# Kernel tuning notes

Hardware: AMD Instinct MI355X
Metric: run time of the kernel (lower is better)

The kernel has to match this reference:

```python
import jax, jax.numpy as jnp
import numpy as np

NINF = -1e5  # large negative used for forbidden transitions (as in partial-tagger)


def setup_inputs() -> dict:
    key = jax.random.key(0)
    ks = jax.random.split(key, 10)
    B, T, H, N = 64, 512, 768, 25
    embeddings = jax.random.normal(ks[0], (B, T, H), jnp.float32)
    lengths = jax.random.randint(ks[1], (B,), T // 2, T + 1)
    mask = jnp.arange(T)[None, :] < lengths[:, None]  # [B,T] bool
    W = jax.random.normal(ks[2], (H, N), jnp.float32) / np.sqrt(H).astype(np.float32)
    b = jnp.zeros((N,), jnp.float32)
    transitions = jax.random.normal(ks[3], (N, N), jnp.float32) * 0.1
    start_transitions = jax.random.normal(ks[4], (N,), jnp.float32) * 0.1
    end_transitions = jax.random.normal(ks[5], (N,), jnp.float32) * 0.1
    start_constraints = (jax.random.uniform(ks[6], (N,)) < 0.7).at[0].set(True)
    end_constraints = (jax.random.uniform(ks[7], (N,)) < 0.7).at[0].set(True)
    transition_constraints = (jax.random.uniform(ks[8], (N, N)) < 0.6) | jnp.eye(N, dtype=bool)
    return dict(embeddings=embeddings, W=W, b=b, transitions=transitions,
                start_transitions=start_transitions, end_transitions=end_transitions,
                mask=mask, start_constraints=start_constraints, end_constraints=end_constraints,
                transition_constraints=transition_constraints, padding_index=0)


def _log_potentials(embeddings, W, b, transitions, start_transitions, end_transitions, mask):
    # emissions [B,T,N]; lp[b,t,k,j] = emit[b,t,j] + trans[k,j]
    B, T, _ = embeddings.shape
    N = transitions.shape[0]
    logits = jnp.einsum('bth,hn->btn', embeddings, W) + b
    lp = logits[:, :, None, :] + transitions[None, None]  # [B,T,N,N]
    first = jnp.broadcast_to((start_transitions + logits[:, 0])[:, None, :], (B, N, N))
    lp = lp.at[:, 0].set(first)
    last_pos = mask.sum(-1) - 1  # [B]
    end_mask = jnp.arange(T)[None, :] == last_pos[:, None]  # [B,T]
    lp = lp + jnp.where(end_mask[:, :, None, None], end_transitions[None, None, None, :], 0.0)
    return lp


def _constrain(lp, mask, start_constraints, end_constraints, transition_constraints):
    B, T, N, _ = lp.shape
    tc = jnp.where(transition_constraints, 0.0, NINF)  # [N,N]
    sc = jnp.where(start_constraints, 0.0, NINF)       # [N]
    ec = jnp.where(end_constraints, 0.0, NINF)         # [N]
    clp = lp + tc[None, None]
    clp = clp.at[:, 0].set(lp[:, 0] + sc[None, None, :])  # start constraint, no transition constraint at t=0
    last_pos = mask.sum(-1) - 1
    end_mask = jnp.arange(T)[None, :] == last_pos[:, None]
    clp = clp + jnp.where(end_mask[:, :, None, None], ec[None, None, None, :], 0.0)
    # padded steps: force a 0-score self transition so they don't affect the path score
    eye = jnp.where(jnp.eye(N, dtype=bool), 0.0, NINF)
    clp = jnp.where(mask[:, :, None, None], clp, eye[None, None])
    return clp


def _viterbi(clp):
    # clp: [B,T,N,N] constrained log potentials -> best tag sequence [B,T]
    clp_t = jnp.swapaxes(clp, 0, 1)  # time-major [T,B,N,N]
    alpha0 = clp_t[0, :, 0, :]  # first-step rows are identical -> take row 0, [B,N]

    def fwd_step(alpha, lp_t):
        scores = alpha[:, :, None] + lp_t  # [B,N,N]
        return jnp.max(scores, axis=1), jnp.argmax(scores, axis=1).astype(jnp.int32)

    alpha_T, backptrs = jax.lax.scan(fwd_step, alpha0, clp_t[1:])  # backptrs [T-1,B,N]
    last_tag = jnp.argmax(alpha_T, axis=-1).astype(jnp.int32)  # [B]

    def bwd_step(tag, bp):
        prev = jnp.take_along_axis(bp, tag[:, None], axis=1).squeeze(1)
        return prev, prev

    _, prevs = jax.lax.scan(bwd_step, last_tag, backptrs, reverse=True)  # [T-1,B]
    tags = jnp.concatenate([prevs, last_tag[None]], axis=0).T  # [B,T]
    return tags


def reference(embeddings, W, b, transitions, start_transitions, end_transitions,
              mask, start_constraints, end_constraints, transition_constraints, padding_index):
    lp = _log_potentials(embeddings, W, b, transitions, start_transitions, end_transitions, mask)
    clp = _constrain(lp, mask, start_constraints, end_constraints, transition_constraints)
    tags = _viterbi(clp)
    out_tags = tags * mask + padding_index * (~mask)
    return lp, out_tags
```

## Files before the change

kernel.cpp:

```cpp
#include <hip/hip_runtime.h>
#include <hip/hip_bf16.h>
#include <stdint.h>

#define NINF -100000.0f

constexpr int Bn = 64, Tn = 512, Hn = 768, Nn = 25;

typedef float float2v __attribute__((ext_vector_type(2)));

__device__ inline float2v pk_mul(float2v a, float2v b) {
    float2v d;
    asm("v_pk_mul_f32 %0, %1, %2" : "=v"(d) : "v"(a), "v"(b));
    return d;
}
__device__ inline float2v pk_add(float2v a, float2v b) {
    float2v d;
    asm("v_pk_add_f32 %0, %1, %2" : "=v"(d) : "v"(a), "v"(b));
    return d;
}

__device__ inline float ldf(const void* p, int i, bool isbf) {
    if (isbf) return __bfloat162float(((const __hip_bfloat16*)p)[i]);
    return ((const float*)p)[i];
}
__device__ inline int ldb(const void* p, int i, int bw) {
    if (bw == 1) return (int)((const uint8_t*)p)[i];
    if (bw == 8) return ((const int*)p)[2 * i];
    return ((const int*)p)[i];
}

__global__ __launch_bounds__(256) void k_prep(
    const void* emb, const void* mask, const void* padidx,
    const void* W, const void* bv, const void* trans, const void* startt, const void* endt,
    const void* sc, const void* ec, const void* tc,
    int* flags, float* wsWf,
    float* wsb, float* wsstart, float* wsend, float* wsscm, float* wsecm,
    float* wstrans, float* wstc, int* lengths)
{
    __shared__ int s_isbf, s_bw;
    __shared__ int ws4[4];
    int blk = blockIdx.x;
    int tid = threadIdx.x;

    if (tid < 64) {
        const uint16_t* e16 = (const uint16_t*)emb;
        uint16_t v = e16[tid];
        int ex = (v >> 7) & 0xFF;
        bool sane = (ex >= 100 && ex <= 140);
        unsigned long long ball = __ballot(sane);
        int cnt = __popcll(ball);
        if (tid == 0) {
            int isbf = (cnt >= 56) ? 1 : 0;
            const int* mw = (const int*)mask;
            int w0 = mw[0];
            int w1 = mw[1];
            int bw;
            if ((unsigned)w0 > 1u) bw = 1;
            else if (w0 == 1 && w1 == 0) bw = 8;
            else bw = 4;
            s_isbf = isbf; s_bw = bw;
            if (blk == 0) {
                flags[0] = isbf;
                flags[1] = bw;
                flags[2] = ((const int*)padidx)[0];
            }
        }
    }
    __syncthreads();
    bool isbf = s_isbf != 0;
    int bw = s_bw;

    {
        int s = (ldb(mask, blk * Tn + tid, bw) ? 1 : 0)
              + (ldb(mask, blk * Tn + 256 + tid, bw) ? 1 : 0);
        for (int off = 32; off; off >>= 1) s += __shfl_down(s, off, 64);
        if ((tid & 63) == 0) ws4[tid >> 6] = s;
        __syncthreads();
        if (tid == 0) lengths[blk] = ws4[0] + ws4[1] + ws4[2] + ws4[3];
    }

    int gid = blk * 256 + tid;
    int gsz = 64 * 256;
    for (int i = gid; i < Hn * Nn; i += gsz) wsWf[i] = ldf(W, i, isbf);
    for (int i = gid; i < Nn; i += gsz) {
        wsb[i]     = ldf(bv, i, isbf);
        wsstart[i] = ldf(startt, i, isbf);
        wsend[i]   = ldf(endt, i, isbf);
        wsscm[i]   = ldb(sc, i, bw) ? 0.0f : NINF;
        wsecm[i]   = ldb(ec, i, bw) ? 0.0f : NINF;
    }
    for (int i = gid; i < Nn * Nn; i += gsz) {
        wstrans[i] = ldf(trans, i, isbf);
        wstc[i]    = ldb(tc, i, bw) ? 0.0f : NINF;
    }
}

__global__ __launch_bounds__(128) void k_gemm(
    const void* embv, const float* wsWf, const float* wsb,
    const int* flags, float* logitsF)
{
    __shared__ float etile[64][65];
    __shared__ float wtile[64][32];
    __shared__ float s_b[25];

    int tid  = threadIdx.x;
    int r    = tid >> 1;
    int half = tid & 1;
    int j0   = half ? 12 : 0;
    int row0 = blockIdx.x * 64;
    int row  = row0 + r;
    bool isbf = flags[0] != 0;

    if (tid < 25) s_b[tid] = wsb[tid];

    float2v acc2[6];
#pragma unroll
    for (int k = 0; k < 6; k++) acc2[k] = (float2v){0.0f, 0.0f};
    float acc12 = 0.0f;

    for (int c = 0; c < 12; c++) {
        __syncthreads();
        if (isbf) {
            const uint16_t* ep = (const uint16_t*)embv;
#pragma unroll
            for (int it = 0; it < 8; it++) {
                int idx = it * 128 + tid;
                int rr = idx >> 4;
                int q  = idx & 15;
                const ushort4* p4 = (const ushort4*)(ep + (size_t)(row0 + rr) * Hn + c * 64);
                ushort4 u = p4[q];
                etile[rr][q * 4 + 0] = __bfloat162float(*(const __hip_bfloat16*)&u.x);
                etile[rr][q * 4 + 1] = __bfloat162float(*(const __hip_bfloat16*)&u.y);
                etile[rr][q * 4 + 2] = __bfloat162float(*(const __hip_bfloat16*)&u.z);
                etile[rr][q * 4 + 3] = __bfloat162float(*(const __hip_bfloat16*)&u.w);
            }
        } else {
            const float* ep = (const float*)embv;
#pragma unroll
            for (int it = 0; it < 8; it++) {
                int idx = it * 128 + tid;
                int rr = idx >> 4;
                int q  = idx & 15;
                const float4* p4 = (const float4*)(ep + (size_t)(row0 + rr) * Hn + c * 64);
                float4 v = p4[q];
                etile[rr][q * 4 + 0] = v.x;
                etile[rr][q * 4 + 1] = v.y;
                etile[rr][q * 4 + 2] = v.z;
                etile[rr][q * 4 + 3] = v.w;
            }
        }
        for (int i = tid; i < 1600; i += 128) {
            int hh = i / 25, j = i - hh * 25;
            wtile[hh][j] = wsWf[(size_t)(c * 64 + hh) * 25 + j];
        }
        __syncthreads();
        {
#pragma clang fp contract(off)
#pragma unroll 4
            for (int hh = 0; hh < 64; hh++) {
                float e = etile[r][hh];
                float2v ee = (float2v){e, e};
                const float4* wp = (const float4*)&wtile[hh][j0];
                float4 w0 = wp[0];
                float4 w1 = wp[1];
                float4 w2 = wp[2];
                float  wl = wtile[hh][j0 + 12];
                acc2[0] = pk_add(acc2[0], pk_mul(ee, (float2v){w0.x, w0.y}));
                acc2[1] = pk_add(acc2[1], pk_mul(ee, (float2v){w0.z, w0.w}));
                acc2[2] = pk_add(acc2[2], pk_mul(ee, (float2v){w1.x, w1.y}));
                acc2[3] = pk_add(acc2[3], pk_mul(ee, (float2v){w1.z, w1.w}));
                acc2[4] = pk_add(acc2[4], pk_mul(ee, (float2v){w2.x, w2.y}));
                acc2[5] = pk_add(acc2[5], pk_mul(ee, (float2v){w2.z, w2.w}));
                acc12 = acc12 + e * wl;
            }
        }
    }

    {
#pragma clang fp contract(off)
#pragma unroll
        for (int p = 0; p < 6; p++) {
            int j = j0 + 2 * p;
            logitsF[(size_t)row * 25 + j]     = acc2[p][0] + s_b[j];
            logitsF[(size_t)row * 25 + j + 1] = acc2[p][1] + s_b[j + 1];
        }
        if (half) logitsF[(size_t)row * 25 + 24] = acc12 + s_b[24];
    }
}

__device__ inline float rdlane(float v, int lane) {
    return __int_as_float(__builtin_amdgcn_readlane(__float_as_int(v), lane));
}
__device__ inline int imin2(int a, int b) { return a < b ? a : b; }

struct SharedV {
    float   lgl[Tn * Nn];
    float   alpha[Tn][26];
    uint8_t bp[511][32];
    uint8_t tags[512];
};
struct SharedL {
    float s_trans[625];
    float s_start[25];
    float s_end[25];
};

__global__ __launch_bounds__(512) void k_tail(
    const float* logitsF, const float* wstrans, const float* wstc,
    const float* wsstart, const float* wsend, const float* wsscm, const float* wsecm,
    const int* lengths, const int* flags, void* out)
{
    __shared__ union { SharedV v; SharedL l; } smem;
    int tid = threadIdx.x;
    bool isbf = flags[0] != 0;

    if (blockIdx.x >= 64) {
        for (int i = tid; i < 625; i += 512) smem.l.s_trans[i] = wstrans[i];
        if (tid < 25) { smem.l.s_start[tid] = wsstart[tid]; smem.l.s_end[tid] = wsend[tid]; }
        __syncthreads();

        int rw0 = (blockIdx.x - 64) * 16;
        int b = rw0 >> 9;
        int last = lengths[b] - 1;
        const float* lg0 = logitsF + (size_t)rw0 * 25;
        size_t obase = (size_t)rw0 * 625;

        for (int idx = tid; idx < 16 * 625; idx += 512) {
            int rr = idx / 625;
            int e  = idx - rr * 625;
            int j  = e % 25;
            int t  = (rw0 + rr) & 511;
            float lg = lg0[rr * 25 + j];
            float v;
            {
#pragma clang fp contract(off)
                if (t == 0) v = smem.l.s_start[j] + lg;
                else        v = lg + smem.l.s_trans[e];
                if (t == last) v += smem.l.s_end[j];
            }
            size_t o = obase + idx;
            if (isbf) ((__hip_bfloat16*)out)[o] = __float2bfloat16(v);
            else      ((float*)out)[o] = v;
        }
        return;
    }

    int b  = blockIdx.x;
    int len  = lengths[b];
    int last = len - 1;
    int padv = flags[2];
    int L   = tid & 63;
    int wid = tid >> 6;
    bool act = (L < 25);
    int j = act ? L : 0;

    {
        const float4* src = (const float4*)(logitsF + (size_t)b * (Tn * Nn));
        float4* dst = (float4*)smem.v.lgl;
        for (int i = tid; i < (Tn * Nn) / 4; i += 512) dst[i] = src[i];
    }

    float tcol[25], tccol[25], ttc[25];
#pragma unroll
    for (int k = 0; k < 25; k++) {
        tcol[k]  = wstrans[k * 25 + j];
        tccol[k] = wstc[k * 25 + j];
        ttc[k] = tcol[k] + tccol[k];
    }
    float endj = wsend[j];
    float ecmj = wsecm[j];

    __syncthreads();

    float areg = 0.0f;
    if (wid == 0) {
        {
#pragma clang fp contract(off)
            areg = (wsstart[j] + smem.v.lgl[j]) + wsscm[j];
        }
        if (act) smem.v.alpha[0][L] = areg;

        float Lg0 = smem.v.lgl[25 + j];
        float Lg1 = smem.v.lgl[imin2(2, last) * 25 + j];

        for (int t = 1; t <= last; ++t) {
            float Lgn = smem.v.lgl[imin2(t + 2, last) * 25 + j];

            float s[25];
            if (t < last) {
#pragma clang fp contract(off)
#pragma unroll
                for (int k = 0; k < 25; k++) {
                    float ak = rdlane(areg, k);
                    s[k] = ak + (Lg0 + ttc[k]);
                }
            } else {
#pragma clang fp contract(off)
#pragma unroll
                for (int k = 0; k < 25; k++) {
                    float ak = rdlane(areg, k);
                    float v = (((Lg0 + tcol[k]) + endj) + tccol[k]) + ecmj;
                    s[k] = ak + v;
                }
            }

            float a0 = fmaxf(fmaxf(s[0],  s[1]),  s[2]);
            float a1 = fmaxf(fmaxf(s[3],  s[4]),  s[5]);
            float a2 = fmaxf(fmaxf(s[6],  s[7]),  s[8]);
            float a3 = fmaxf(fmaxf(s[9],  s[10]), s[11]);
            float a4 = fmaxf(fmaxf(s[12], s[13]), s[14]);
            float a5 = fmaxf(fmaxf(s[15], s[16]), s[17]);
            float a6 = fmaxf(fmaxf(s[18], s[19]), s[20]);
            float a7 = fmaxf(fmaxf(s[21], s[22]), s[23]);
            float b0 = fmaxf(fmaxf(a0, a1), a2);
            float b1 = fmaxf(fmaxf(a3, a4), a5);
            float b2 = fmaxf(fmaxf(a6, a7), s[24]);
            float m  = fmaxf(fmaxf(b0, b1), b2);

            areg = m;
            if (act) smem.v.alpha[t][L] = m;
            Lg0 = Lg1; Lg1 = Lgn;
        }
    }
    __syncthreads();

    for (int t = 1 + wid; t <= last; t += 8) {
        float ap = smem.v.alpha[t - 1][j];
        float mj = smem.v.alpha[t][j];
        float Lg = smem.v.lgl[t * 25 + j];

        float s[25];
        if (t < last) {
#pragma clang fp contract(off)
#pragma unroll
            for (int k = 0; k < 25; k++) {
                float ak = rdlane(ap, k);
                s[k] = ak + (Lg + ttc[k]);
            }
        } else {
#pragma clang fp contract(off)
#pragma unroll
            for (int k = 0; k < 25; k++) {
                float ak = rdlane(ap, k);
                float v = (((Lg + tcol[k]) + endj) + tccol[k]) + ecmj;
                s[k] = ak + v;
            }
        }

        int ik[25];
#pragma unroll
        for (int k = 0; k < 25; k++) ik[k] = (s[k] == mj) ? k : 32;
        int q0 = imin2(imin2(ik[0],  ik[1]),  ik[2]);
        int q1 = imin2(imin2(ik[3],  ik[4]),  ik[5]);
        int q2 = imin2(imin2(ik[6],  ik[7]),  ik[8]);
        int q3 = imin2(imin2(ik[9],  ik[10]), ik[11]);
        int q4 = imin2(imin2(ik[12], ik[13]), ik[14]);
        int q5 = imin2(imin2(ik[15], ik[16]), ik[17]);
        int q6 = imin2(imin2(ik[18], ik[19]), ik[20]);
        int q7 = imin2(imin2(ik[21], ik[22]), ik[23]);
        int r0 = imin2(imin2(q0, q1), q2);
        int r1 = imin2(imin2(q3, q4), q5);
        int r2 = imin2(imin2(q6, q7), ik[24]);
        int mi = imin2(imin2(r0, r1), r2);

        if (act) smem.v.bp[t - 1][L] = (uint8_t)mi;
    }
    __syncthreads();

    if (wid == 0) {
        float am = rdlane(areg, 0);
        int ami = 0;
#pragma unroll
        for (int k = 1; k < 25; k++) {
            float v2 = rdlane(areg, k);
            bool g = v2 > am;
            am  = g ? v2 : am;
            ami = g ? k  : ami;
        }
        int tag = ami;
        if (L == 0) smem.v.tags[last] = (uint8_t)tag;

        int Lc = L & 31;
        int k2 = last - 1;
        while (k2 >= 7) {
            int c0 = smem.v.bp[k2    ][Lc];
            int c1 = smem.v.bp[k2 - 1][Lc];
            int c2 = smem.v.bp[k2 - 2][Lc];
            int c3 = smem.v.bp[k2 - 3][Lc];
            int c4 = smem.v.bp[k2 - 4][Lc];
            int c5 = smem.v.bp[k2 - 5][Lc];
            int c6 = smem.v.bp[k2 - 6][Lc];
            int c7 = smem.v.bp[k2 - 7][Lc];
            tag = __builtin_amdgcn_readlane(c0, tag); if (L == 0) smem.v.tags[k2    ] = (uint8_t)tag;
            tag = __builtin_amdgcn_readlane(c1, tag); if (L == 0) smem.v.tags[k2 - 1] = (uint8_t)tag;
            tag = __builtin_amdgcn_readlane(c2, tag); if (L == 0) smem.v.tags[k2 - 2] = (uint8_t)tag;
            tag = __builtin_amdgcn_readlane(c3, tag); if (L == 0) smem.v.tags[k2 - 3] = (uint8_t)tag;
            tag = __builtin_amdgcn_readlane(c4, tag); if (L == 0) smem.v.tags[k2 - 4] = (uint8_t)tag;
            tag = __builtin_amdgcn_readlane(c5, tag); if (L == 0) smem.v.tags[k2 - 5] = (uint8_t)tag;
            tag = __builtin_amdgcn_readlane(c6, tag); if (L == 0) smem.v.tags[k2 - 6] = (uint8_t)tag;
            tag = __builtin_amdgcn_readlane(c7, tag); if (L == 0) smem.v.tags[k2 - 7] = (uint8_t)tag;
            k2 -= 8;
        }
        while (k2 >= 0) {
            int c = smem.v.bp[k2][Lc];
            tag = __builtin_amdgcn_readlane(c, tag);
            if (L == 0) smem.v.tags[k2] = (uint8_t)tag;
            k2--;
        }
    }
    __syncthreads();

    size_t base = 20480000ull;
    for (int t = tid; t < 512; t += 512) {
        float val = (t < len) ? (float)smem.v.tags[t] : (float)padv;
        size_t o = base + (size_t)b * 512 + t;
        if (isbf) ((__hip_bfloat16*)out)[o] = __float2bfloat16(val);
        else      ((float*)out)[o] = val;
    }
}

extern "C" void kernel_launch(void* const* d_in, const int* in_sizes, int n_in,
                              void* d_out, int out_size, void* d_ws, size_t ws_size,
                              hipStream_t stream) {
    const void* emb  = d_in[0];
    const void* W    = d_in[1];
    const void* bv   = d_in[2];
    const void* tr   = d_in[3];
    const void* st   = d_in[4];
    const void* en   = d_in[5];
    const void* mask = d_in[6];
    const void* sc   = d_in[7];
    const void* ec   = d_in[8];
    const void* tc   = d_in[9];
    const void* pad  = d_in[10];

    char* ws = (char*)d_ws;
    int*    flags    = (int*)ws;
    int*    lengths  = (int*)(ws + 64);
    float*  wsb      = (float*)(ws + 384);
    float*  wsstart  = (float*)(ws + 512);
    float*  wsend    = (float*)(ws + 640);
    float*  wsscm    = (float*)(ws + 768);
    float*  wsecm    = (float*)(ws + 896);
    float*  wstrans  = (float*)(ws + 1024);
    float*  wstc     = (float*)(ws + 3584);
    float*  wsWf     = (float*)(ws + 6144);
    float*  logitsF  = (float*)(ws + 82944);

    k_prep<<<64, 256, 0, stream>>>(emb, mask, pad, W, bv, tr, st, en, sc, ec, tc,
                                   flags, wsWf, wsb, wsstart, wsend, wsscm, wsecm,
                                   wstrans, wstc, lengths);
    k_gemm<<<512, 128, 0, stream>>>(emb, wsWf, wsb, flags, logitsF);
    k_tail<<<2112, 512, 0, stream>>>(logitsF, wstrans, wstc, wsstart, wsend,
                                     wsscm, wsecm, lengths, flags, d_out);
}
```

Before: 415.0 us.

## Fuse prep and GEMM kernels into one launch and unroll Viterbi forward loop

Merges the separate prep kernel into the GEMM kernel. Extra blocks now compute lengths, flags and constraint tables, and the GEMM blocks read W and bias straight from the inputs instead of a converted workspace copy. This removes one kernel launch and a dependency round-trip. The Viterbi forward recursion is restructured into batches of 8 steps with the emission loads hoisted and the final step peeled out of the loop, and the LDS tile stores and loads are vectorised to float4. The cost is that W is converted redundantly in every GEMM block, and the tail kernel still reads lengths and flags written by the same fused kernel, which relies on the stream order.

```diff
diff --git a/kernel.cpp b/kernel.cpp
--- a/kernel.cpp
+++ b/kernel.cpp
@@ -19,7 +19,7 @@
     return d;
 }
 
-__device__ inline float ldf(const void* p, int i, bool isbf) {
+__device__ inline float ldf(const void* p, size_t i, bool isbf) {
     if (isbf) return __bfloat162float(((const __hip_bfloat16*)p)[i]);
     return ((const float*)p)[i];
 }
@@ -29,89 +29,112 @@
     return ((const int*)p)[i];
 }
 
-__global__ __launch_bounds__(256) void k_prep(
-    const void* emb, const void* mask, const void* padidx,
+__device__ inline float rdlane(float v, int lane) {
+    return __int_as_float(__builtin_amdgcn_readlane(__float_as_int(v), lane));
+}
+__device__ inline int imin2(int a, int b) { return a < b ? a : b; }
+
+__device__ inline float amax25(const float* s) {
+    float a0 = fmaxf(fmaxf(s[0],  s[1]),  s[2]);
+    float a1 = fmaxf(fmaxf(s[3],  s[4]),  s[5]);
+    float a2 = fmaxf(fmaxf(s[6],  s[7]),  s[8]);
+    float a3 = fmaxf(fmaxf(s[9],  s[10]), s[11]);
+    float a4 = fmaxf(fmaxf(s[12], s[13]), s[14]);
+    float a5 = fmaxf(fmaxf(s[15], s[16]), s[17]);
+    float a6 = fmaxf(fmaxf(s[18], s[19]), s[20]);
+    float a7 = fmaxf(fmaxf(s[21], s[22]), s[23]);
+    float b0 = fmaxf(fmaxf(a0, a1), a2);
+    float b1 = fmaxf(fmaxf(a3, a4), a5);
+    float b2 = fmaxf(fmaxf(a6, a7), s[24]);
+    return fmaxf(fmaxf(b0, b1), b2);
+}
+
+__device__ inline float stepx(float areg, float Lg, const float* ttc) {
+    float s[25];
+    {
+#pragma clang fp contract(off)
+#pragma unroll
+        for (int k = 0; k < 25; k++) {
+            float ak = rdlane(areg, k);
+            s[k] = ak + (Lg + ttc[k]);
+        }
+    }
+    return amax25(s);
+}
+
+__global__ __launch_bounds__(128) void k_front(
+    const void* embv, const void* mask, const void* padidx,
     const void* W, const void* bv, const void* trans, const void* startt, const void* endt,
     const void* sc, const void* ec, const void* tc,
-    int* flags, float* wsWf,
-    float* wsb, float* wsstart, float* wsend, float* wsscm, float* wsecm,
-    float* wstrans, float* wstc, int* lengths)
+    int* flags, float* wstrans, float* wstc,
+    float* wsstart, float* wsend, float* wsscm, float* wsecm,
+    int* lengths, float* logitsF)
 {
-    __shared__ int s_isbf, s_bw;
-    __shared__ int ws4[4];
-    int blk = blockIdx.x;
+    __shared__ float etile[64][76];
+    __shared__ float wtile[64][32];
+    __shared__ float s_b[25];
+    __shared__ int   s_isbf;
+    __shared__ int   ws2[2];
+
     int tid = threadIdx.x;
+    int bid = blockIdx.x;
 
     if (tid < 64) {
-        const uint16_t* e16 = (const uint16_t*)emb;
+        const uint16_t* e16 = (const uint16_t*)embv;
         uint16_t v = e16[tid];
         int ex = (v >> 7) & 0xFF;
         bool sane = (ex >= 100 && ex <= 140);
         unsigned long long ball = __ballot(sane);
-        int cnt = __popcll(ball);
-        if (tid == 0) {
-            int isbf = (cnt >= 56) ? 1 : 0;
-            const int* mw = (const int*)mask;
-            int w0 = mw[0];
-            int w1 = mw[1];
-            int bw;
-            if ((unsigned)w0 > 1u) bw = 1;
-            else if (w0 == 1 && w1 == 0) bw = 8;
-            else bw = 4;
-            s_isbf = isbf; s_bw = bw;
-            if (blk == 0) {
-                flags[0] = isbf;
-                flags[1] = bw;
-                flags[2] = ((const int*)padidx)[0];
-            }
-        }
+        if (tid == 0) s_isbf = (__popcll(ball) >= 56) ? 1 : 0;
     }
     __syncthreads();
     bool isbf = s_isbf != 0;
-    int bw = s_bw;
-
-    {
-        int s = (ldb(mask, blk * Tn + tid, bw) ? 1 : 0)
-              + (ldb(mask, blk * Tn + 256 + tid, bw) ? 1 : 0);
-        for (int off = 32; off; off >>= 1) s += __shfl_down(s, off, 64);
-        if ((tid & 63) == 0) ws4[tid >> 6] = s;
-        __syncthreads();
-        if (tid == 0) lengths[blk] = ws4[0] + ws4[1] + ws4[2] + ws4[3];
-    }
-
-    int gid = blk * 256 + tid;
-    int gsz = 64 * 256;
-    for (int i = gid; i < Hn * Nn; i += gsz) wsWf[i] = ldf(W, i, isbf);
-    for (int i = gid; i < Nn; i += gsz) {
-        wsb[i]     = ldf(bv, i, isbf);
-        wsstart[i] = ldf(startt, i, isbf);
-        wsend[i]   = ldf(endt, i, isbf);
-        wsscm[i]   = ldb(sc, i, bw) ? 0.0f : NINF;
-        wsecm[i]   = ldb(ec, i, bw) ? 0.0f : NINF;
-    }
-    for (int i = gid; i < Nn * Nn; i += gsz) {
-        wstrans[i] = ldf(trans, i, isbf);
-        wstc[i]    = ldb(tc, i, bw) ? 0.0f : NINF;
-    }
-}
-
-__global__ __launch_bounds__(128) void k_gemm(
-    const void* embv, const float* wsWf, const float* wsb,
-    const int* flags, float* logitsF)
-{
-    __shared__ float etile[64][65];
-    __shared__ float wtile[64][32];
-    __shared__ float s_b[25];
-
-    int tid  = threadIdx.x;
+
+    if (bid >= 512) {
+        int pb = bid - 512;
+        const int* mw = (const int*)mask;
+        int w0 = mw[0], w1 = mw[1];
+        int bw;
+        if ((unsigned)w0 > 1u) bw = 1;
+        else if (w0 == 1 && w1 == 0) bw = 8;
+        else bw = 4;
+        if (pb == 0 && tid == 0) {
+            flags[0] = isbf ? 1 : 0;
+            flags[1] = bw;
+            flags[2] = ((const int*)padidx)[0];
+        }
+        {
+            int s = 0;
+#pragma unroll
+            for (int u = 0; u < 4; u++)
+                s += (ldb(mask, pb * Tn + u * 128 + tid, bw) ? 1 : 0);
+            for (int off = 32; off; off >>= 1) s += __shfl_down(s, off, 64);
+            if ((tid & 63) == 0) ws2[tid >> 6] = s;
+            __syncthreads();
+            if (tid == 0) lengths[pb] = ws2[0] + ws2[1];
+        }
+        int gid = pb * 128 + tid;
+        int gsz = 64 * 128;
+        for (int i = gid; i < Nn; i += gsz) {
+            wsstart[i] = ldf(startt, i, isbf);
+            wsend[i]   = ldf(endt, i, isbf);
+            wsscm[i]   = ldb(sc, i, bw) ? 0.0f : NINF;
+            wsecm[i]   = ldb(ec, i, bw) ? 0.0f : NINF;
+        }
+        for (int i = gid; i < Nn * Nn; i += gsz) {
+            wstrans[i] = ldf(trans, i, isbf);
+            wstc[i]    = ldb(tc, i, bw) ? 0.0f : NINF;
+        }
+        return;
+    }
+
     int r    = tid >> 1;
     int half = tid & 1;
     int j0   = half ? 12 : 0;
-    int row0 = blockIdx.x * 64;
+    int row0 = bid * 64;
     int row  = row0 + r;
-    bool isbf = flags[0] != 0;
-
-    if (tid < 25) s_b[tid] = wsb[tid];
+
+    if (tid < 25) s_b[tid] = ldf(bv, tid, isbf);
 
     float2v acc2[6];
 #pragma unroll
@@ -129,10 +152,12 @@
                 int q  = idx & 15;
                 const ushort4* p4 = (const ushort4*)(ep + (size_t)(row0 + rr) * Hn + c * 64);
                 ushort4 u = p4[q];
-                etile[rr][q * 4 + 0] = __bfloat162float(*(const __hip_bfloat16*)&u.x);
-                etile[rr][q * 4 + 1] = __bfloat162float(*(const __hip_bfloat16*)&u.y);
-                etile[rr][q * 4 + 2] = __bfloat162float(*(const __hip_bfloat16*)&u.z);
-                etile[rr][q * 4 + 3] = __bfloat162float(*(const __hip_bfloat16*)&u.w);
+                float4 f;
+                f.x = __bfloat162float(*(const __hip_bfloat16*)&u.x);
+                f.y = __bfloat162float(*(const __hip_bfloat16*)&u.y);
+                f.z = __bfloat162float(*(const __hip_bfloat16*)&u.z);
+                f.w = __bfloat162float(*(const __hip_bfloat16*)&u.w);
+                *(float4*)&etile[rr][q * 4] = f;
             }
         } else {
             const float* ep = (const float*)embv;
@@ -142,36 +167,36 @@
                 int rr = idx >> 4;
                 int q  = idx & 15;
                 const float4* p4 = (const float4*)(ep + (size_t)(row0 + rr) * Hn + c * 64);
-                float4 v = p4[q];
-                etile[rr][q * 4 + 0] = v.x;
-                etile[rr][q * 4 + 1] = v.y;
-                etile[rr][q * 4 + 2] = v.z;
-                etile[rr][q * 4 + 3] = v.w;
+                *(float4*)&etile[rr][q * 4] = p4[q];
             }
         }
         for (int i = tid; i < 1600; i += 128) {
-            int hh = i / 25, j = i - hh * 25;
-            wtile[hh][j] = wsWf[(size_t)(c * 64 + hh) * 25 + j];
+            int hh = i / 25, jj = i - hh * 25;
+            wtile[hh][jj] = ldf(W, (size_t)c * 1600 + i, isbf);
         }
         __syncthreads();
         {
 #pragma clang fp contract(off)
-#pragma unroll 4
-            for (int hh = 0; hh < 64; hh++) {
-                float e = etile[r][hh];
-                float2v ee = (float2v){e, e};
-                const float4* wp = (const float4*)&wtile[hh][j0];
-                float4 w0 = wp[0];
-                float4 w1 = wp[1];
-                float4 w2 = wp[2];
-                float  wl = wtile[hh][j0 + 12];
-                acc2[0] = pk_add(acc2[0], pk_mul(ee, (float2v){w0.x, w0.y}));
-                acc2[1] = pk_add(acc2[1], pk_mul(ee, (float2v){w0.z, w0.w}));
-                acc2[2] = pk_add(acc2[2], pk_mul(ee, (float2v){w1.x, w1.y}));
-                acc2[3] = pk_add(acc2[3], pk_mul(ee, (float2v){w1.z, w1.w}));
-                acc2[4] = pk_add(acc2[4], pk_mul(ee, (float2v){w2.x, w2.y}));
-                acc2[5] = pk_add(acc2[5], pk_mul(ee, (float2v){w2.z, w2.w}));
-                acc12 = acc12 + e * wl;
+            for (int h4 = 0; h4 < 16; h4++) {
+                float4 e4 = *(const float4*)&etile[r][h4 * 4];
+#pragma unroll
+                for (int u = 0; u < 4; u++) {
+                    int hh = h4 * 4 + u;
+                    float e = (u == 0) ? e4.x : (u == 1) ? e4.y : (u == 2) ? e4.z : e4.w;
+                    float2v ee = (float2v){e, e};
+                    const float4* wp = (const float4*)&wtile[hh][j0];
+                    float4 w0 = wp[0];
+                    float4 w1 = wp[1];
+                    float4 w2 = wp[2];
+                    float  wl = wtile[hh][j0 + 12];
+                    acc2[0] = pk_add(acc2[0], pk_mul(ee, (float2v){w0.x, w0.y}));
+                    acc2[1] = pk_add(acc2[1], pk_mul(ee, (float2v){w0.z, w0.w}));
+                    acc2[2] = pk_add(acc2[2], pk_mul(ee, (float2v){w1.x, w1.y}));
+                    acc2[3] = pk_add(acc2[3], pk_mul(ee, (float2v){w1.z, w1.w}));
+                    acc2[4] = pk_add(acc2[4], pk_mul(ee, (float2v){w2.x, w2.y}));
+                    acc2[5] = pk_add(acc2[5], pk_mul(ee, (float2v){w2.z, w2.w}));
+                    acc12 = acc12 + e * wl;
+                }
             }
         }
     }
@@ -187,11 +212,6 @@
         if (half) logitsF[(size_t)row * 25 + 24] = acc12 + s_b[24];
     }
 }
-
-__device__ inline float rdlane(float v, int lane) {
-    return __int_as_float(__builtin_amdgcn_readlane(__float_as_int(v), lane));
-}
-__device__ inline int imin2(int a, int b) { return a < b ? a : b; }
 
 struct SharedV {
     float   lgl[Tn * Nn];
@@ -280,46 +300,39 @@
         }
         if (act) smem.v.alpha[0][L] = areg;
 
-        float Lg0 = smem.v.lgl[25 + j];
-        float Lg1 = smem.v.lgl[imin2(2, last) * 25 + j];
-
-        for (int t = 1; t <= last; ++t) {
-            float Lgn = smem.v.lgl[imin2(t + 2, last) * 25 + j];
-
+        int tEndX = last - 1;
+        int t = 1;
+        for (; t + 7 <= tEndX; t += 8) {
+            float Lg8[8];
+#pragma unroll
+            for (int u = 0; u < 8; u++) Lg8[u] = smem.v.lgl[(t + u) * 25 + j];
+            float a8[8];
+#pragma unroll
+            for (int u = 0; u < 8; u++) { areg = stepx(areg, Lg8[u], ttc); a8[u] = areg; }
+            if (act) {
+#pragma unroll
+                for (int u = 0; u < 8; u++) smem.v.alpha[t + u][L] = a8[u];
+            }
+        }
+        for (; t <= tEndX; ++t) {
+            float Lg = smem.v.lgl[t * 25 + j];
+            areg = stepx(areg, Lg, ttc);
+            if (act) smem.v.alpha[t][L] = areg;
+        }
+        {
+            float Lg = smem.v.lgl[last * 25 + j];
             float s[25];
-            if (t < last) {
+            {
 #pragma clang fp contract(off)
 #pragma unroll
                 for (int k = 0; k < 25; k++) {
                     float ak = rdlane(areg, k);
-                    s[k] = ak + (Lg0 + ttc[k]);
-                }
-            } else {
-#pragma clang fp contract(off)
-#pragma unroll
-                for (int k = 0; k < 25; k++) {
-                    float ak = rdlane(areg, k);
-                    float v = (((Lg0 + tcol[k]) + endj) + tccol[k]) + ecmj;
+                    float v = (((Lg + tcol[k]) + endj) + tccol[k]) + ecmj;
                     s[k] = ak + v;
                 }
             }
-
-            float a0 = fmaxf(fmaxf(s[0],  s[1]),  s[2]);
-            float a1 = fmaxf(fmaxf(s[3],  s[4]),  s[5]);
-            float a2 = fmaxf(fmaxf(s[6],  s[7]),  s[8]);
-            float a3 = fmaxf(fmaxf(s[9],  s[10]), s[11]);
-            float a4 = fmaxf(fmaxf(s[12], s[13]), s[14]);
-            float a5 = fmaxf(fmaxf(s[15], s[16]), s[17]);
-            float a6 = fmaxf(fmaxf(s[18], s[19]), s[20]);
-            float a7 = fmaxf(fmaxf(s[21], s[22]), s[23]);
-            float b0 = fmaxf(fmaxf(a0, a1), a2);
-            float b1 = fmaxf(fmaxf(a3, a4), a5);
-            float b2 = fmaxf(fmaxf(a6, a7), s[24]);
-            float m  = fmaxf(fmaxf(b0, b1), b2);
-
-            areg = m;
-            if (act) smem.v.alpha[t][L] = m;
-            Lg0 = Lg1; Lg1 = Lgn;
+            areg = amax25(s);
+            if (act) smem.v.alpha[last][L] = areg;
         }
     }
     __syncthreads();
@@ -411,7 +424,8 @@
     __syncthreads();
 
     size_t base = 20480000ull;
-    for (int t = tid; t < 512; t += 512) {
+    {
+        int t = tid;
         float val = (t < len) ? (float)smem.v.tags[t] : (float)padv;
         size_t o = base + (size_t)b * 512 + t;
         if (isbf) ((__hip_bfloat16*)out)[o] = __float2bfloat16(val);
@@ -437,20 +451,17 @@
     char* ws = (char*)d_ws;
     int*    flags    = (int*)ws;
     int*    lengths  = (int*)(ws + 64);
-    float*  wsb      = (float*)(ws + 384);
     float*  wsstart  = (float*)(ws + 512);
     float*  wsend    = (float*)(ws + 640);
     float*  wsscm    = (float*)(ws + 768);
     float*  wsecm    = (float*)(ws + 896);
     float*  wstrans  = (float*)(ws + 1024);
     float*  wstc     = (float*)(ws + 3584);
-    float*  wsWf     = (float*)(ws + 6144);
     float*  logitsF  = (float*)(ws + 82944);
 
-    k_prep<<<64, 256, 0, stream>>>(emb, mask, pad, W, bv, tr, st, en, sc, ec, tc,
-                                   flags, wsWf, wsb, wsstart, wsend, wsscm, wsecm,
-                                   wstrans, wstc, lengths);
-    k_gemm<<<512, 128, 0, stream>>>(emb, wsWf, wsb, flags, logitsF);
+    k_front<<<576, 128, 0, stream>>>(emb, mask, pad, W, bv, tr, st, en, sc, ec, tc,
+                                     flags, wstrans, wstc, wsstart, wsend, wsscm, wsecm,
+                                     lengths, logitsF);
     k_tail<<<2112, 512, 0, stream>>>(logitsF, wstrans, wstc, wsstart, wsend,
                                      wsscm, wsecm, lengths, flags, d_out);
 }
```

Result: no change. 419.1 us (+1.0%).
